# Kernel optimization log

Hardware: AMD Instinct MI355X
Metric: run time of the kernel (lower is better)

The kernel has to match this reference:

```python
import jax, jax.numpy as jnp
import numpy as np

V = 100000
E = 524288
D_IN = 128
D_OUT = 128
NUM_REL = 474
BN_EPS = 1e-5


def setup_inputs() -> dict:
    key = jax.random.key(0)
    ks = jax.random.split(key, 12)
    return {
        "x": jax.random.normal(ks[0], (V, D_IN), dtype=jnp.float32),
        "rel_repr": jax.random.normal(ks[1], (NUM_REL, D_IN), dtype=jnp.float32),
        "edge_norm": jax.random.uniform(ks[2], (E,), dtype=jnp.float32),
        "in_w": jax.random.normal(ks[3], (D_IN, D_OUT), dtype=jnp.float32) * 0.1,
        "out_w": jax.random.normal(ks[4], (D_IN, D_OUT), dtype=jnp.float32) * 0.1,
        "loop_w": jax.random.normal(ks[5], (D_IN, D_OUT), dtype=jnp.float32) * 0.1,
        "w_rel": jax.random.normal(ks[6], (D_IN, D_OUT), dtype=jnp.float32) * 0.1,
        "loop_rel": jax.random.normal(ks[7], (1, D_IN), dtype=jnp.float32),
        "bias": jnp.zeros((D_OUT,), dtype=jnp.float32),
        "src": jax.random.randint(ks[8], (E,), 0, V, dtype=jnp.int32),
        "dst": jax.random.randint(ks[9], (E,), 0, V, dtype=jnp.int32),
        "edge_type": jax.random.randint(ks[10], (E,), 0, NUM_REL, dtype=jnp.int32),
    }


def reference(x, rel_repr, edge_norm, in_w, out_w, loop_w, w_rel, loop_rel, bias, src, dst, edge_type):
    # comp primitive 'mult': edge_data = src_emb * rel[edge_type]   [E, D_IN]
    rel = rel_repr  # num_base=-1 -> rel_wt is None, rel.data = rel_repr
    edge_data = x[src] * rel[edge_type]
    half = edge_data.shape[0] // 2  # static under jit
    # first half of edges -> in_w, second half -> out_w
    msg = jnp.concatenate([edge_data[:half] @ in_w, edge_data[half:] @ out_w], axis=0)
    msg = msg * edge_norm[:, None]
    # agg primitive 'sum': scatter-sum into dst nodes
    agg = jax.ops.segment_sum(msg, dst, num_segments=x.shape[0])  # [V, D_OUT]
    # self-loop path: comp(x, loop_rel) @ loop_w
    loop_msg = (x * loop_rel) @ loop_w
    # comb primitive 'add', scaled by 1/3 (dropout with p=0 is identity)
    h = (agg + loop_msg) * (1.0 / 3.0)
    h = h + bias
    # BatchNorm1d, training-mode batch stats, gamma=1, beta=0
    mean = jnp.mean(h, axis=0)
    var = jnp.mean((h - mean) ** 2, axis=0)
    h = (h - mean) * jax.lax.rsqrt(var + BN_EPS)
    # act primitive 'relu'; ltr=True -> project relations
    return jax.nn.relu(h), rel @ w_rel
```

## Files before the change

kernel.cpp:

```cpp
#include <hip/hip_runtime.h>

#define V 100000
#define VP 100096
#define E_EDGES 524288
#define HALF 262144
#define D 128
#define NREL 474
#define BN_EPS 1e-5f
#define NBLK 98

#define ROWTILES 782
#define RED_BLKS 98
#define RELB 237
#define BNBLK 12500

#define LDK 392
#define LDB 40

typedef unsigned short u16;
typedef unsigned int u32;
typedef unsigned long long u64;
typedef __attribute__((ext_vector_type(8))) short short8;
typedef __attribute__((ext_vector_type(4))) float f32x4;

__device__ __forceinline__ u16 f2bf(float f) {
    union { float f; u32 u; } v; v.f = f;
    u32 u = v.u;
    return (u16)((u + 0x7fffu + ((u >> 16) & 1u)) >> 16);
}
__device__ __forceinline__ u32 pk2(float a, float b) {
    return (u32)f2bf(a) | ((u32)f2bf(b) << 16);
}

__global__ __launch_bounds__(256) void hist_k(const int* __restrict__ dst, u32* __restrict__ cnt) {
    int e = blockIdx.x * 256 + threadIdx.x;
    if (e >= E_EDGES) return;
    u32 d = (u32)dst[e];
    if (d >= V) d = 0;
    atomicAdd(&cnt[d], 1u);
}

__global__ __launch_bounds__(1024) void scanA_k(const u32* __restrict__ cnt,
                                                u32* __restrict__ cursor,
                                                u32* __restrict__ bsum) {
    __shared__ u32 wsum[16];
    int tid = threadIdx.x, wid = tid >> 6, lane = tid & 63;
    int idx = blockIdx.x * 1024 + tid;
    u32 v = (idx < V) ? cnt[idx] : 0u;
    u32 s = v;
#pragma unroll
    for (int o = 1; o < 64; o <<= 1) {
        u32 t = __shfl_up(s, o, 64);
        if (lane >= o) s += t;
    }
    if (lane == 63) wsum[wid] = s;
    __syncthreads();
    if (wid == 0) {
        u32 wv = (lane < 16) ? wsum[lane] : 0u;
#pragma unroll
        for (int o = 1; o < 16; o <<= 1) {
            u32 t = __shfl_up(wv, o, 64);
            if (lane >= o) wv += t;
        }
        if (lane < 16) wsum[lane] = wv;
    }
    __syncthreads();
    u32 wprev = wid ? wsum[wid - 1] : 0u;
    if (idx < V) cursor[idx] = s + wprev - v;
    if (tid == 0) bsum[blockIdx.x] = wsum[15];
}

__global__ __launch_bounds__(128) void scanB_k(u32* __restrict__ bsum) {
    __shared__ u32 wtot;
    int t = threadIdx.x, lane = t & 63, w = t >> 6;
    u32 v = (t < NBLK) ? bsum[t] : 0u;
    u32 s = v;
#pragma unroll
    for (int o = 1; o < 64; o <<= 1) {
        u32 x = __shfl_up(s, o, 64);
        if (lane >= o) s += x;
    }
    if (w == 0 && lane == 63) wtot = s;
    __syncthreads();
    u32 add = (w == 1) ? wtot : 0u;
    if (t < NBLK) bsum[t] = add + s - v;
}

__global__ __launch_bounds__(256) void fill_rec_k(
    const int* __restrict__ dst, const int* __restrict__ src, const int* __restrict__ etype,
    const float* __restrict__ enorm, u32* __restrict__ cursor, const u32* __restrict__ bsum,
    u64* __restrict__ rec) {
    int e = blockIdx.x * 256 + threadIdx.x;
    if (e >= E_EDGES) return;
    u32 d = (u32)dst[e];   if (d >= V) d = 0;
    u32 s = (u32)src[e];   if (s >= V) s = 0;
    u32 t = (u32)etype[e]; if (t >= NREL) t = 0;
    float nm = enorm[e];
    u32 w = s | (t << 17) | ((e < HALF ? 0u : 1u) << 26);
    u32 slot = atomicAdd(&cursor[d], 1u) + bsum[d >> 10];
    u64 r = (u64)w | ((u64)__float_as_uint(nm) << 32);
    if (slot < E_EDGES) rec[slot] = r;
}

struct Rec { u32 s, t, hf; float nm; };
__device__ __forceinline__ Rec dec(u64 r) {
    Rec q; u32 w = (u32)r;
    q.s = w & 0x1FFFFu;          if (q.s >= V) q.s = 0;
    q.t = (w >> 17) & 0x1FFu;    if (q.t >= NREL) q.t = 0;
    q.hf = (w >> 26) & 1u;
    q.nm = __uint_as_float((u32)(r >> 32));
    return q;
}

__global__ __launch_bounds__(256) void gather_k(
    const float* __restrict__ x, const float* __restrict__ rel,
    const u32* __restrict__ cursor, const u32* __restrict__ cnt,
    const u32* __restrict__ bsum, const u64* __restrict__ rec, u16* __restrict__ Aagg) {
    int wave = threadIdx.x >> 6, lane = threadIdx.x & 63;
    int v = blockIdx.x * 4 + wave;
    if (v >= VP) return;
    u32* arow = (u32*)(Aagg + (size_t)v * 256);
    if (v >= V) { arow[lane] = 0u; arow[64 + lane] = 0u; return; }

    u32 n = cnt[v];
    u32 end = cursor[v] + bsum[v >> 10];
    if (end > E_EDGES) end = E_EDGES;
    if (n > end) n = end;
    u32 p = end - n;
    int col = lane * 2;

    float iA0 = 0.f, iA1 = 0.f, oA0 = 0.f, oA1 = 0.f;
    float iB0 = 0.f, iB1 = 0.f, oB0 = 0.f, oB1 = 0.f;

    u64 rb0 = 0, rb1 = 0, rb2 = 0, rb3 = 0;
    if (p     < end) rb0 = rec[p];
    if (p + 1 < end) rb1 = rec[p + 1];
    if (p + 2 < end) rb2 = rec[p + 2];
    if (p + 3 < end) rb3 = rec[p + 3];

    for (u32 q = p; q < end; q += 4) {
        u64 rn0 = 0, rn1 = 0, rn2 = 0, rn3 = 0;
        if (q + 4 < end) rn0 = rec[q + 4];
        if (q + 5 < end) rn1 = rec[q + 5];
        if (q + 6 < end) rn2 = rec[q + 6];
        if (q + 7 < end) rn3 = rec[q + 7];

        Rec q0 = dec(rb0), q1 = dec(rb1), q2 = dec(rb2), q3 = dec(rb3);
        float2 x0 = *(const float2*)(x + (size_t)q0.s * D + col);
        float2 x1 = *(const float2*)(x + (size_t)q1.s * D + col);
        float2 x2 = *(const float2*)(x + (size_t)q2.s * D + col);
        float2 x3 = *(const float2*)(x + (size_t)q3.s * D + col);
        float2 v0 = *(const float2*)(rel + (size_t)q0.t * D + col);
        float2 v1 = *(const float2*)(rel + (size_t)q1.t * D + col);
        float2 v2 = *(const float2*)(rel + (size_t)q2.t * D + col);
        float2 v3 = *(const float2*)(rel + (size_t)q3.t * D + col);
        float f00 = x0.x * v0.x * q0.nm, f01 = x0.y * v0.y * q0.nm;
        float f10 = x1.x * v1.x * q1.nm, f11 = x1.y * v1.y * q1.nm;
        float f20 = x2.x * v2.x * q2.nm, f21 = x2.y * v2.y * q2.nm;
        float f30 = x3.x * v3.x * q3.nm, f31 = x3.y * v3.y * q3.nm;
        if (q0.hf) { oA0 += f00; oA1 += f01; } else { iA0 += f00; iA1 += f01; }
        if (q1.hf) { oB0 += f10; oB1 += f11; } else { iB0 += f10; iB1 += f11; }
        if (q2.hf) { oA0 += f20; oA1 += f21; } else { iA0 += f20; iA1 += f21; }
        if (q3.hf) { oB0 += f30; oB1 += f31; } else { iB0 += f30; iB1 += f31; }

        rb0 = rn0; rb1 = rn1; rb2 = rn2; rb3 = rn3;
    }
    arow[lane]      = pk2(iA0 + iB0, iA1 + iB1);
    arow[64 + lane] = pk2(oA0 + oB0, oA1 + oB1);
}

__global__ __launch_bounds__(128) void bt_k(
    const float* __restrict__ in_w, const float* __restrict__ out_w,
    const float* __restrict__ loop_w, u16* __restrict__ Bt) {
    int n = blockIdx.x;
    int t = threadIdx.x;
    const float* Ws[3] = {in_w, out_w, loop_w};
#pragma unroll
    for (int seg = 0; seg < 3; seg++)
        Bt[(size_t)n * 384 + seg * 128 + t] = f2bf(Ws[seg][(size_t)t * D + n]);
}

__global__ __launch_bounds__(512) void gemm_k(
    const u16* __restrict__ Aagg, const u16* __restrict__ Bt,
    const float* __restrict__ x, const float* __restrict__ loop_rel,
    float* __restrict__ h_out, float* __restrict__ psum, float* __restrict__ psq) {
    __shared__ u16 Bs[64 * 384];
    __shared__ float s_sum[64], s_sq[64];
    int tid = threadIdx.x, wave = tid >> 6, lane = tid & 63;
    int half = blockIdx.x & 1;
    int rt   = blockIdx.x >> 1;
    int row0 = rt * 128;

    if (tid < 64) s_sum[tid] = 0.f;
    else if (tid < 128) s_sq[tid - 64] = 0.f;

    int m16 = lane & 15;
    int kq = (lane >> 4) * 8;
    int gvm = row0 + wave * 16 + m16;
    const u16* arow = Aagg + (size_t)gvm * 256;
    bool vok = gvm < V;

    short8 af[8];
#pragma unroll
    for (int ks = 0; ks < 8; ks++) af[ks] = *(const short8*)(arow + ks * 32 + kq);
    float4 xf[8];
    {
        const float* xp = x + (size_t)gvm * D + kq;
#pragma unroll
        for (int kk = 0; kk < 4; kk++) {
            xf[2 * kk]     = vok ? *(const float4*)(xp + kk * 32)     : (float4){0.f, 0.f, 0.f, 0.f};
            xf[2 * kk + 1] = vok ? *(const float4*)(xp + kk * 32 + 4) : (float4){0.f, 0.f, 0.f, 0.f};
        }
    }

    {
        const u16* srcB = Bt + (size_t)half * 64 * 384;
        char* bsb = (char*)Bs;
#pragma unroll
        for (int it = 0; it < 6; it++) {
            int c = it * 512 + tid;
            int n = c / 48, s = c - n * 48;
            short8 vv = *(const short8*)(srcB + (size_t)n * 384 + s * 8);
            *(short8*)(bsb + (((u32)(n * 768 + s * 16)) ^ (u32)((n & 7) << 4))) = vv;
        }
    }
    __syncthreads();

    const char* bsb = (const char*)Bs;
    f32x4 acc[4];
#pragma unroll
    for (int ct = 0; ct < 4; ct++) acc[ct] = (f32x4){0.f, 0.f, 0.f, 0.f};

#pragma unroll
    for (int ks = 0; ks < 8; ks++) {
#pragma unroll
        for (int ct = 0; ct < 4; ct++) {
            int n = ct * 16 + m16;
            short8 b = *(const short8*)(bsb + (((u32)(n * 768 + (ks * 32 + kq) * 2)) ^ (u32)((n & 7) << 4)));
            acc[ct] = __builtin_amdgcn_mfma_f32_16x16x32_bf16(af[ks], b, acc[ct], 0, 0, 0);
        }
    }
#pragma unroll
    for (int kk = 0; kk < 4; kk++) {
        float4 l0 = *(const float4*)(loop_rel + kk * 32 + kq);
        float4 l1 = *(const float4*)(loop_rel + kk * 32 + kq + 4);
        float4 x0 = xf[2 * kk], x1 = xf[2 * kk + 1];
        union { u32 u[4]; short8 s; } c;
        c.u[0] = pk2(x0.x * l0.x, x0.y * l0.y);
        c.u[1] = pk2(x0.z * l0.z, x0.w * l0.w);
        c.u[2] = pk2(x1.x * l1.x, x1.y * l1.y);
        c.u[3] = pk2(x1.z * l1.z, x1.w * l1.w);
#pragma unroll
        for (int ct = 0; ct < 4; ct++) {
            int n = ct * 16 + m16;
            short8 b = *(const short8*)(bsb + (((u32)(n * 768 + (256 + kk * 32 + kq) * 2)) ^ (u32)((n & 7) << 4)));
            acc[ct] = __builtin_amdgcn_mfma_f32_16x16x32_bf16(c.s, b, acc[ct], 0, 0, 0);
        }
    }

    int m4 = (lane >> 4) * 4;
#pragma unroll
    for (int ct = 0; ct < 4; ct++) {
        float ls = 0.f, lq = 0.f;
#pragma unroll
        for (int i = 0; i < 4; i++) {
            int gv = row0 + wave * 16 + m4 + i;
            if (gv < V) {
                float h = acc[ct][i] * (1.0f / 3.0f);
                h_out[(size_t)gv * D + half * 64 + ct * 16 + m16] = h;
                ls += h; lq += h * h;
            }
        }
        atomicAdd(&s_sum[ct * 16 + m16], ls);
        atomicAdd(&s_sq[ct * 16 + m16], lq);
    }
    __syncthreads();
    if (tid < 64) psum[(size_t)rt * 128 + half * 64 + tid] = s_sum[tid];
    else if (tid < 128) psq[(size_t)rt * 128 + half * 64 + (tid - 64)] = s_sq[tid - 64];
}

__global__ __launch_bounds__(256) void bn_reduce(
    const float* __restrict__ psum, const float* __restrict__ psq,
    float* __restrict__ colsum, float* __restrict__ colsumsq) {
    int t = threadIdx.x;
    int c = t & 127;
    const float* srcp = (t < 128) ? psum : psq;
    float s = 0.f;
    int r0 = blockIdx.x * 8;
#pragma unroll
    for (int i = 0; i < 8; i++) {
        int r = r0 + i;
        if (r < ROWTILES) s += srcp[(size_t)r * 128 + c];
    }
    atomicAdd(((t < 128) ? colsum : colsumsq) + c, s);
}

__global__ __launch_bounds__(256) void final_k(
    float* __restrict__ hio, const float* __restrict__ colsum, const float* __restrict__ colsumsq,
    const float* __restrict__ rel, const float* __restrict__ w, float* __restrict__ out1) {
    int bid = blockIdx.x;
    if (bid < RELB) {
        __shared__ float rs[2][D];
        int rh = threadIdx.x >> 7, c = threadIdx.x & 127;
        int r = bid * 2 + rh;
        rs[rh][c] = rel[(size_t)r * D + c];
        __syncthreads();
        float s = 0.f;
#pragma unroll 8
        for (int k = 0; k < D; k++) s += rs[rh][k] * w[(size_t)k * D + c];
        out1[(size_t)r * D + c] = s;
        return;
    }
    int idx = ((bid - RELB) * 256 + threadIdx.x) * 4;
    if (idx >= V * D) return;
    int col = idx & (D - 1);
    float4 hv = *(const float4*)(hio + idx);
    float4 ov;
    {
        float m0 = colsum[col + 0] * (1.0f / (float)V);
        float m1 = colsum[col + 1] * (1.0f / (float)V);
        float m2 = colsum[col + 2] * (1.0f / (float)V);
        float m3 = colsum[col + 3] * (1.0f / (float)V);
        if (!isfinite(m0)) m0 = 0.f;
        if (!isfinite(m1)) m1 = 0.f;
        if (!isfinite(m2)) m2 = 0.f;
        if (!isfinite(m3)) m3 = 0.f;
        float v0 = colsumsq[col + 0] * (1.0f / (float)V) - m0 * m0;
        float v1 = colsumsq[col + 1] * (1.0f / (float)V) - m1 * m1;
        float v2 = colsumsq[col + 2] * (1.0f / (float)V) - m2 * m2;
        float v3 = colsumsq[col + 3] * (1.0f / (float)V) - m3 * m3;
        if (!isfinite(v0) || v0 < 0.f) v0 = 0.f;
        if (!isfinite(v1) || v1 < 0.f) v1 = 0.f;
        if (!isfinite(v2) || v2 < 0.f) v2 = 0.f;
        if (!isfinite(v3) || v3 < 0.f) v3 = 0.f;
        float f0 = (hv.x - m0) * rsqrtf(v0 + BN_EPS);
        float f1 = (hv.y - m1) * rsqrtf(v1 + BN_EPS);
        float f2 = (hv.z - m2) * rsqrtf(v2 + BN_EPS);
        float f3 = (hv.w - m3) * rsqrtf(v3 + BN_EPS);
        ov.x = (f0 > 0.f) ? f0 : 0.f;
        ov.y = (f1 > 0.f) ? f1 : 0.f;
        ov.z = (f2 > 0.f) ? f2 : 0.f;
        ov.w = (f3 > 0.f) ? f3 : 0.f;
    }
    *(float4*)(hio + idx) = ov;
}

__global__ __launch_bounds__(1024) void scan_k(const u32* __restrict__ cnt,
                                               u32* __restrict__ cursor) {
    __shared__ u32 wsum[16];
    __shared__ u32 carry_s;
    int tid = threadIdx.x, wid = tid >> 6, lane = tid & 63;
    if (tid == 0) carry_s = 0;
    __syncthreads();
    for (int base = 0; base < V; base += 1024) {
        int idx = base + tid;
        u32 v = (idx < V) ? cnt[idx] : 0u;
        u32 s = v;
#pragma unroll
        for (int o = 1; o < 64; o <<= 1) {
            u32 t = __shfl_up(s, o, 64);
            if (lane >= o) s += t;
        }
        if (lane == 63) wsum[wid] = s;
        __syncthreads();
        if (wid == 0) {
            u32 wv = (lane < 16) ? wsum[lane] : 0u;
#pragma unroll
            for (int o = 1; o < 16; o <<= 1) {
                u32 t = __shfl_up(wv, o, 64);
                if (lane >= o) wv += t;
            }
            if (lane < 16) wsum[lane] = wv;
        }
        __syncthreads();
        u32 wprev = (wid == 0) ? 0u : wsum[wid - 1];
        u32 c = carry_s;
        if (idx < V) cursor[idx] = c + s + wprev - v;
        u32 tot = wsum[15];
        __syncthreads();
        if (tid == 0) carry_s = c + tot;
        __syncthreads();
    }
}

__global__ __launch_bounds__(256) void fill_k(
    const int* __restrict__ dst, u32* __restrict__ cursor, u32* __restrict__ eid) {
    int e = blockIdx.x * 256 + threadIdx.x;
    if (e >= E_EDGES) return;
    u32 d = (u32)dst[e];
    if (d >= V) d = 0;
    u32 slot = atomicAdd(&cursor[d], 1u);
    if (slot < E_EDGES) eid[slot] = (u32)e;
}

__global__ __launch_bounds__(256, 1) void fused_k(
    const float* __restrict__ x, const float* __restrict__ rel, const float* __restrict__ loop_rel,
    const float* __restrict__ in_w, const float* __restrict__ out_w, const float* __restrict__ loop_w,
    const float* __restrict__ enorm,
    const int* __restrict__ src, const int* __restrict__ etype,
    const u32* __restrict__ cursor, const u32* __restrict__ cnt,
    const u32* __restrict__ eid,
    float* __restrict__ h_out, float* __restrict__ colsum, float* __restrict__ colsumsq) {
    __shared__ u16 Alds[64 * LDK];
    __shared__ u16 Bs[D * LDB];
    __shared__ float s_sum[D], s_sq[D];

    int tid = threadIdx.x, wave = tid >> 6, lane = tid & 63;
    int row0 = blockIdx.x * 64;

    if (tid < D) { s_sum[tid] = 0.f; s_sq[tid] = 0.f; }

    for (int i = 0; i < 16; i++) {
        int row = wave * 16 + i;
        int gv = row0 + row;
        u32* arow = (u32*)(Alds + row * LDK);
        if (gv < V) {
            float a0 = 0.f, a1 = 0.f, b0 = 0.f, b1 = 0.f;
            float c0 = 0.f, c1 = 0.f, d0 = 0.f, d1 = 0.f;
            u32 n = cnt[gv];
            u32 end = cursor[gv];
            u32 beg = (end >= n) ? end - n : 0u;
            if (beg >= E_EDGES) { beg = 0; n = 0; }
            if (n > E_EDGES - beg) n = E_EDGES - beg;
            u32 nend = beg + n;
            u32 p = beg;
            for (; p + 2 <= nend; p += 2) {
                u32 e0 = eid[p];           if (e0 >= E_EDGES) e0 = 0;
                u32 e1 = eid[p + 1];       if (e1 >= E_EDGES) e1 = 0;
                u32 s0 = (u32)src[e0];     if (s0 >= V) s0 = 0;
                u32 s1 = (u32)src[e1];     if (s1 >= V) s1 = 0;
                u32 t0 = (u32)etype[e0];   if (t0 >= NREL) t0 = 0;
                u32 t1 = (u32)etype[e1];   if (t1 >= NREL) t1 = 0;
                float n0 = enorm[e0];
                float n1 = enorm[e1];
                float2 xv0 = *(const float2*)(x + (size_t)s0 * D + lane * 2);
                float2 xv1 = *(const float2*)(x + (size_t)s1 * D + lane * 2);
                float2 rv0 = *(const float2*)(rel + (size_t)t0 * D + lane * 2);
                float2 rv1 = *(const float2*)(rel + (size_t)t1 * D + lane * 2);
                float f00 = xv0.x * rv0.x * n0, f01 = xv0.y * rv0.y * n0;
                float f10 = xv1.x * rv1.x * n1, f11 = xv1.y * rv1.y * n1;
                if (e0 < HALF) { a0 += f00; a1 += f01; } else { b0 += f00; b1 += f01; }
                if (e1 < HALF) { c0 += f10; c1 += f11; } else { d0 += f10; d1 += f11; }
            }
            if (p < nend) {
                u32 e0 = eid[p];           if (e0 >= E_EDGES) e0 = 0;
                u32 s0 = (u32)src[e0];     if (s0 >= V) s0 = 0;
                u32 t0 = (u32)etype[e0];   if (t0 >= NREL) t0 = 0;
                float n0 = enorm[e0];
                float2 xv0 = *(const float2*)(x + (size_t)s0 * D + lane * 2);
                float2 rv0 = *(const float2*)(rel + (size_t)t0 * D + lane * 2);
                float f00 = xv0.x * rv0.x * n0, f01 = xv0.y * rv0.y * n0;
                if (e0 < HALF) { a0 += f00; a1 += f01; } else { b0 += f00; b1 += f01; }
            }
            a0 += c0; a1 += c1; b0 += d0; b1 += d1;
            float2 xv = *(const float2*)(x + (size_t)gv * D + lane * 2);
            float2 lv = *(const float2*)(loop_rel + lane * 2);
            arow[lane]       = pk2(a0, a1);
            arow[64 + lane]  = pk2(b0, b1);
            arow[128 + lane] = pk2(xv.x * lv.x, xv.y * lv.y);
        } else {
            arow[lane] = 0u; arow[64 + lane] = 0u; arow[128 + lane] = 0u;
        }
    }
    __syncthreads();

    f32x4 acc[8];
#pragma unroll
    for (int ct = 0; ct < 8; ct++) acc[ct] = (f32x4){0.f, 0.f, 0.f, 0.f};

    int m = wave * 16 + (lane & 15);
    int kq = (lane >> 4) * 8;
    int bk = tid >> 3;
    int bn0 = (tid & 7) * 16;

    for (int ks = 0; ks < 12; ks++) {
        int k0 = ks * 32;
        int seg = k0 >> 7;
        int kloc = k0 & 127;
        const float* W = (seg == 0) ? in_w : (seg == 1 ? out_w : loop_w);
#pragma unroll
        for (int j = 0; j < 16; j += 2) {
            float2 w2 = *(const float2*)(W + (size_t)(kloc + bk) * D + bn0 + j);
            Bs[(bn0 + j) * LDB + bk]     = f2bf(w2.x);
            Bs[(bn0 + j + 1) * LDB + bk] = f2bf(w2.y);
        }
        __syncthreads();
        short8 a = *(const short8*)(Alds + m * LDK + k0 + kq);
#pragma unroll
        for (int ct = 0; ct < 8; ct++) {
            short8 b = *(const short8*)(Bs + (ct * 16 + (lane & 15)) * LDB + kq);
            acc[ct] = __builtin_amdgcn_mfma_f32_16x16x32_bf16(a, b, acc[ct], 0, 0, 0);
        }
        __syncthreads();
    }

    int m4 = (lane >> 4) * 4;
#pragma unroll
    for (int ct = 0; ct < 8; ct++) {
        float ls = 0.f, lq = 0.f;
#pragma unroll
        for (int i = 0; i < 4; i++) {
            int gv = row0 + wave * 16 + m4 + i;
            if (gv < V) {
                float h = acc[ct][i] * (1.0f / 3.0f);
                h_out[(size_t)gv * D + ct * 16 + (lane & 15)] = h;
                ls += h; lq += h * h;
            }
        }
        atomicAdd(&s_sum[ct * 16 + (lane & 15)], ls);
        atomicAdd(&s_sq[ct * 16 + (lane & 15)], lq);
    }
    __syncthreads();
    if (tid < D) atomicAdd(&colsum[tid], s_sum[tid]);
    else atomicAdd(&colsumsq[tid - D], s_sq[tid - D]);
}

__global__ void bn_finalize(const float* __restrict__ colsum, const float* __restrict__ colsumsq,
                            float* __restrict__ mean, float* __restrict__ scale) {
    int t = threadIdx.x;
    float m = colsum[t] * (1.0f / (float)V);
    if (!isfinite(m)) m = 0.f;
    float var = colsumsq[t] * (1.0f / (float)V) - m * m;
    if (!isfinite(var) || var < 0.f) var = 0.f;
    mean[t] = m;
    scale[t] = rsqrtf(var + BN_EPS);
}

__global__ __launch_bounds__(256) void bn_relu(
    float* __restrict__ hio, const float* __restrict__ mean, const float* __restrict__ scale) {
    int idx = (blockIdx.x * 256 + threadIdx.x) * 4;
    if (idx >= V * D) return;
    int col = idx & (D - 1);
    float4 hv = *(const float4*)(hio + idx);
    float f0 = (hv.x - mean[col + 0]) * scale[col + 0];
    float f1 = (hv.y - mean[col + 1]) * scale[col + 1];
    float f2 = (hv.z - mean[col + 2]) * scale[col + 2];
    float f3 = (hv.w - mean[col + 3]) * scale[col + 3];
    f0 = (f0 > 0.f) ? f0 : 0.f;
    f1 = (f1 > 0.f) ? f1 : 0.f;
    f2 = (f2 > 0.f) ? f2 : 0.f;
    f3 = (f3 > 0.f) ? f3 : 0.f;
    float4 ov; ov.x = f0; ov.y = f1; ov.z = f2; ov.w = f3;
    *(float4*)(hio + idx) = ov;
}

__global__ __launch_bounds__(128) void rel_gemm(
    const float* __restrict__ rel, const float* __restrict__ w, float* __restrict__ out1) {
    __shared__ float rs[D];
    int t = threadIdx.x;
    int r = blockIdx.x;
    rs[t] = rel[(size_t)r * D + t];
    __syncthreads();
    float s = 0.f;
#pragma unroll 8
    for (int k = 0; k < D; k++) s += rs[k] * w[(size_t)k * D + t];
    out1[(size_t)r * D + t] = s;
}

extern "C" void kernel_launch(void* const* d_in, const int* in_sizes, int n_in,
                              void* d_out, int out_size, void* d_ws, size_t ws_size,
                              hipStream_t stream) {
    const float* x        = (const float*)d_in[0];
    const float* rel_repr = (const float*)d_in[1];
    const float* enorm    = (const float*)d_in[2];
    const float* in_w     = (const float*)d_in[3];
    const float* out_w    = (const float*)d_in[4];
    const float* loop_w   = (const float*)d_in[5];
    const float* w_rel    = (const float*)d_in[6];
    const float* loop_rel = (const float*)d_in[7];
    const int* src   = (const int*)d_in[9];
    const int* dst   = (const int*)d_in[10];
    const int* etype = (const int*)d_in[11];

    float* out0 = (float*)d_out;
    float* out1 = (float*)d_out + (size_t)V * D;

    char* ws = (char*)d_ws;

    {
        size_t off = 0;
        u32* cnt        = (u32*)(ws + off); off += (size_t)V * 4;
        float* colsum   = (float*)(ws + off); off += 512;
        float* colsumsq = (float*)(ws + off); off += 512;
        size_t zero_bytes = off;
        u32* cursor = (u32*)(ws + off); off += (size_t)V * 4;
        u32* bsum   = (u32*)(ws + off); off += 512;
        u16* Bt     = (u16*)(ws + off); off += (size_t)128 * 384 * 2;
        float* psum = (float*)(ws + off); off += (size_t)ROWTILES * 128 * 4;
        float* psq  = (float*)(ws + off); off += (size_t)ROWTILES * 128 * 4;
        u64* rec    = (u64*)(ws + off); off += (size_t)E_EDGES * 8;
        u16* Aagg   = (u16*)(ws + off); off += (size_t)VP * 256 * 2;

        if (ws_size >= off) {
            hipMemsetAsync(d_ws, 0, zero_bytes, stream);
            bt_k<<<128, 128, 0, stream>>>(in_w, out_w, loop_w, Bt);
            hist_k<<<(E_EDGES + 255) / 256, 256, 0, stream>>>(dst, cnt);
            scanA_k<<<NBLK, 1024, 0, stream>>>(cnt, cursor, bsum);
            scanB_k<<<1, 128, 0, stream>>>(bsum);
            fill_rec_k<<<(E_EDGES + 255) / 256, 256, 0, stream>>>(dst, src, etype, enorm, cursor, bsum, rec);
            gather_k<<<VP / 4, 256, 0, stream>>>(x, rel_repr, cursor, cnt, bsum, rec, Aagg);
            gemm_k<<<ROWTILES * 2, 512, 0, stream>>>(Aagg, Bt, x, loop_rel, out0, psum, psq);
            bn_reduce<<<RED_BLKS, 256, 0, stream>>>(psum, psq, colsum, colsumsq);
            final_k<<<RELB + BNBLK, 256, 0, stream>>>(out0, colsum, colsumsq, rel_repr, w_rel, out1);
            return;
        }
    }

    {
        size_t off = 0;
        u32* cnt      = (u32*)(ws + off); off += (size_t)V * 4;
        float* colsum = (float*)(ws + off); off += 512;
        float* colsumsq = (float*)(ws + off); off += 512;
        size_t zero_bytes = off;
        u32* cursor   = (u32*)(ws + off); off += (size_t)V * 4;
        float* meanp  = (float*)(ws + off); off += 512;
        float* scalep = (float*)(ws + off); off += 512;
        u32* eid      = (u32*)(ws + off); off += (size_t)E_EDGES * 4;

        if (ws_size < off) return;

        hipMemsetAsync(d_ws, 0, zero_bytes, stream);
        hist_k<<<(E_EDGES + 255) / 256, 256, 0, stream>>>(dst, cnt);
        scan_k<<<1, 1024, 0, stream>>>(cnt, cursor);
        fill_k<<<(E_EDGES + 255) / 256, 256, 0, stream>>>(dst, cursor, eid);
        fused_k<<<(V + 63) / 64, 256, 0, stream>>>(x, rel_repr, loop_rel, in_w, out_w, loop_w,
                                                   enorm, src, etype,
                                                   cursor, cnt, eid,
                                                   out0, colsum, colsumsq);
        bn_finalize<<<1, 128, 0, stream>>>(colsum, colsumsq, meanp, scalep);
        bn_relu<<<(V * D / 4 + 255) / 256, 256, 0, stream>>>(out0, meanp, scalep);
        rel_gemm<<<NREL, 128, 0, stream>>>(rel_repr, w_rel, out1);
    }
}
```

Before: 335.1 us.

## Fuse weight transpose into scan kernel, simplify gather loads, remap GEMM blocks

```diff
diff --git a/kernel.cpp b/kernel.cpp
--- a/kernel.cpp
+++ b/kernel.cpp
@@ -10,6 +10,7 @@
 #define NBLK 98
 
 #define ROWTILES 782
+#define GEMM_GRID 1568
 #define RED_BLKS 98
 #define RELB 237
 #define BNBLK 12500
@@ -70,7 +71,19 @@
     if (tid == 0) bsum[blockIdx.x] = wsum[15];
 }
 
-__global__ __launch_bounds__(128) void scanB_k(u32* __restrict__ bsum) {
+__global__ __launch_bounds__(128) void scanBbt_k(
+    u32* __restrict__ bsum,
+    const float* __restrict__ in_w, const float* __restrict__ out_w,
+    const float* __restrict__ loop_w, u16* __restrict__ Bt) {
+    if (blockIdx.x > 0) {
+        int n = blockIdx.x - 1;
+        int t = threadIdx.x;
+        const float* Ws[3] = {in_w, out_w, loop_w};
+#pragma unroll
+        for (int seg = 0; seg < 3; seg++)
+            Bt[(size_t)n * 384 + seg * 128 + t] = f2bf(Ws[seg][(size_t)t * D + n]);
+        return;
+    }
     __shared__ u32 wtot;
     int t = threadIdx.x, lane = t & 63, w = t >> 6;
     u32 v = (t < NBLK) ? bsum[t] : 0u;
@@ -105,8 +118,8 @@
 struct Rec { u32 s, t, hf; float nm; };
 __device__ __forceinline__ Rec dec(u64 r) {
     Rec q; u32 w = (u32)r;
-    q.s = w & 0x1FFFFu;          if (q.s >= V) q.s = 0;
-    q.t = (w >> 17) & 0x1FFu;    if (q.t >= NREL) q.t = 0;
+    q.s = w & 0x1FFFFu;
+    q.t = (w >> 17) & 0x1FFu;
     q.hf = (w >> 26) & 1u;
     q.nm = __uint_as_float((u32)(r >> 32));
     return q;
@@ -118,7 +131,6 @@
     const u32* __restrict__ bsum, const u64* __restrict__ rec, u16* __restrict__ Aagg) {
     int wave = threadIdx.x >> 6, lane = threadIdx.x & 63;
     int v = blockIdx.x * 4 + wave;
-    if (v >= VP) return;
     u32* arow = (u32*)(Aagg + (size_t)v * 256);
     if (v >= V) { arow[lane] = 0u; arow[64 + lane] = 0u; return; }
 
@@ -132,20 +144,12 @@
     float iA0 = 0.f, iA1 = 0.f, oA0 = 0.f, oA1 = 0.f;
     float iB0 = 0.f, iB1 = 0.f, oB0 = 0.f, oB1 = 0.f;
 
-    u64 rb0 = 0, rb1 = 0, rb2 = 0, rb3 = 0;
-    if (p     < end) rb0 = rec[p];
-    if (p + 1 < end) rb1 = rec[p + 1];
-    if (p + 2 < end) rb2 = rec[p + 2];
-    if (p + 3 < end) rb3 = rec[p + 3];
-
     for (u32 q = p; q < end; q += 4) {
-        u64 rn0 = 0, rn1 = 0, rn2 = 0, rn3 = 0;
-        if (q + 4 < end) rn0 = rec[q + 4];
-        if (q + 5 < end) rn1 = rec[q + 5];
-        if (q + 6 < end) rn2 = rec[q + 6];
-        if (q + 7 < end) rn3 = rec[q + 7];
-
-        Rec q0 = dec(rb0), q1 = dec(rb1), q2 = dec(rb2), q3 = dec(rb3);
+        u64 r0 = rec[q], r1 = rec[q + 1], r2 = rec[q + 2], r3 = rec[q + 3];
+        Rec q0 = dec(r0), q1 = dec(r1), q2 = dec(r2), q3 = dec(r3);
+        if (q + 1 >= end) q1.nm = 0.f;
+        if (q + 2 >= end) q2.nm = 0.f;
+        if (q + 3 >= end) q3.nm = 0.f;
         float2 x0 = *(const float2*)(x + (size_t)q0.s * D + col);
         float2 x1 = *(const float2*)(x + (size_t)q1.s * D + col);
         float2 x2 = *(const float2*)(x + (size_t)q2.s * D + col);
@@ -162,22 +166,9 @@
         if (q1.hf) { oB0 += f10; oB1 += f11; } else { iB0 += f10; iB1 += f11; }
         if (q2.hf) { oA0 += f20; oA1 += f21; } else { iA0 += f20; iA1 += f21; }
         if (q3.hf) { oB0 += f30; oB1 += f31; } else { iB0 += f30; iB1 += f31; }
-
-        rb0 = rn0; rb1 = rn1; rb2 = rn2; rb3 = rn3;
     }
     arow[lane]      = pk2(iA0 + iB0, iA1 + iB1);
     arow[64 + lane] = pk2(oA0 + oB0, oA1 + oB1);
-}
-
-__global__ __launch_bounds__(128) void bt_k(
-    const float* __restrict__ in_w, const float* __restrict__ out_w,
-    const float* __restrict__ loop_w, u16* __restrict__ Bt) {
-    int n = blockIdx.x;
-    int t = threadIdx.x;
-    const float* Ws[3] = {in_w, out_w, loop_w};
-#pragma unroll
-    for (int seg = 0; seg < 3; seg++)
-        Bt[(size_t)n * 384 + seg * 128 + t] = f2bf(Ws[seg][(size_t)t * D + n]);
 }
 
 __global__ __launch_bounds__(512) void gemm_k(
@@ -187,8 +178,10 @@
     __shared__ u16 Bs[64 * 384];
     __shared__ float s_sum[64], s_sq[64];
     int tid = threadIdx.x, wave = tid >> 6, lane = tid & 63;
-    int half = blockIdx.x & 1;
-    int rt   = blockIdx.x >> 1;
+    int bid = blockIdx.x;
+    int rt   = ((bid >> 4) << 3) | (bid & 7);
+    int half = (bid >> 3) & 1;
+    if (rt >= ROWTILES) return;
     int row0 = rt * 128;
 
     if (tid < 64) s_sum[tid] = 0.f;
@@ -203,25 +196,33 @@
     short8 af[8];
 #pragma unroll
     for (int ks = 0; ks < 8; ks++) af[ks] = *(const short8*)(arow + ks * 32 + kq);
-    float4 xf[8];
+    short8 lf[4];
     {
         const float* xp = x + (size_t)gvm * D + kq;
 #pragma unroll
         for (int kk = 0; kk < 4; kk++) {
-            xf[2 * kk]     = vok ? *(const float4*)(xp + kk * 32)     : (float4){0.f, 0.f, 0.f, 0.f};
-            xf[2 * kk + 1] = vok ? *(const float4*)(xp + kk * 32 + 4) : (float4){0.f, 0.f, 0.f, 0.f};
+            float4 x0 = vok ? *(const float4*)(xp + kk * 32)     : (float4){0.f, 0.f, 0.f, 0.f};
+            float4 x1 = vok ? *(const float4*)(xp + kk * 32 + 4) : (float4){0.f, 0.f, 0.f, 0.f};
+            float4 l0 = *(const float4*)(loop_rel + kk * 32 + kq);
+            float4 l1 = *(const float4*)(loop_rel + kk * 32 + kq + 4);
+            union { u32 u[4]; short8 s; } c;
+            c.u[0] = pk2(x0.x * l0.x, x0.y * l0.y);
+            c.u[1] = pk2(x0.z * l0.z, x0.w * l0.w);
+            c.u[2] = pk2(x1.x * l1.x, x1.y * l1.y);
+            c.u[3] = pk2(x1.z * l1.z, x1.w * l1.w);
+            lf[kk] = c.s;
         }
     }
 
     {
         const u16* srcB = Bt + (size_t)half * 64 * 384;
-        char* bsb = (char*)Bs;
+        char* bsw = (char*)Bs;
 #pragma unroll
         for (int it = 0; it < 6; it++) {
             int c = it * 512 + tid;
             int n = c / 48, s = c - n * 48;
             short8 vv = *(const short8*)(srcB + (size_t)n * 384 + s * 8);
-            *(short8*)(bsb + (((u32)(n * 768 + s * 16)) ^ (u32)((n & 7) << 4))) = vv;
+            *(short8*)(bsw + (((u32)(n * 768 + s * 16)) ^ (u32)((n & 7) << 4))) = vv;
         }
     }
     __syncthreads();
@@ -242,19 +243,11 @@
     }
 #pragma unroll
     for (int kk = 0; kk < 4; kk++) {
-        float4 l0 = *(const float4*)(loop_rel + kk * 32 + kq);
-        float4 l1 = *(const float4*)(loop_rel + kk * 32 + kq + 4);
-        float4 x0 = xf[2 * kk], x1 = xf[2 * kk + 1];
-        union { u32 u[4]; short8 s; } c;
-        c.u[0] = pk2(x0.x * l0.x, x0.y * l0.y);
-        c.u[1] = pk2(x0.z * l0.z, x0.w * l0.w);
-        c.u[2] = pk2(x1.x * l1.x, x1.y * l1.y);
-        c.u[3] = pk2(x1.z * l1.z, x1.w * l1.w);
 #pragma unroll
         for (int ct = 0; ct < 4; ct++) {
             int n = ct * 16 + m16;
             short8 b = *(const short8*)(bsb + (((u32)(n * 768 + (256 + kk * 32 + kq) * 2)) ^ (u32)((n & 7) << 4)));
-            acc[ct] = __builtin_amdgcn_mfma_f32_16x16x32_bf16(c.s, b, acc[ct], 0, 0, 0);
+            acc[ct] = __builtin_amdgcn_mfma_f32_16x16x32_bf16(lf[kk], b, acc[ct], 0, 0, 0);
         }
     }
 
@@ -588,18 +581,18 @@
         u16* Bt     = (u16*)(ws + off); off += (size_t)128 * 384 * 2;
         float* psum = (float*)(ws + off); off += (size_t)ROWTILES * 128 * 4;
         float* psq  = (float*)(ws + off); off += (size_t)ROWTILES * 128 * 4;
-        u64* rec    = (u64*)(ws + off); off += (size_t)E_EDGES * 8;
+        u64* rec    = (u64*)(ws + off); off += (size_t)(E_EDGES + 8) * 8;
         u16* Aagg   = (u16*)(ws + off); off += (size_t)VP * 256 * 2;
 
         if (ws_size >= off) {
             hipMemsetAsync(d_ws, 0, zero_bytes, stream);
-            bt_k<<<128, 128, 0, stream>>>(in_w, out_w, loop_w, Bt);
+            hipMemsetAsync(rec + E_EDGES, 0, 64, stream);
             hist_k<<<(E_EDGES + 255) / 256, 256, 0, stream>>>(dst, cnt);
             scanA_k<<<NBLK, 1024, 0, stream>>>(cnt, cursor, bsum);
-            scanB_k<<<1, 128, 0, stream>>>(bsum);
+            scanBbt_k<<<129, 128, 0, stream>>>(bsum, in_w, out_w, loop_w, Bt);
             fill_rec_k<<<(E_EDGES + 255) / 256, 256, 0, stream>>>(dst, src, etype, enorm, cursor, bsum, rec);
             gather_k<<<VP / 4, 256, 0, stream>>>(x, rel_repr, cursor, cnt, bsum, rec, Aagg);
-            gemm_k<<<ROWTILES * 2, 512, 0, stream>>>(Aagg, Bt, x, loop_rel, out0, psum, psq);
+            gemm_k<<<GEMM_GRID, 512, 0, stream>>>(Aagg, Bt, x, loop_rel, out0, psum, psq);
             bn_reduce<<<RED_BLKS, 256, 0, stream>>>(psum, psq, colsum, colsumsq);
             final_k<<<RELB + BNBLK, 256, 0, stream>>>(out0, colsum, colsumsq, rel_repr, w_rel, out1);
             return;
```

Result: faster. 319.9 us (-4.5%).
